# Kernel optimization log

Measured on AMD Instinct MI355X. Metric: run time of the kernel, lower is better.

The kernel has to match this reference:

```python
import jax, jax.numpy as jnp
import numpy as np


def conv3x3(x, w, b):
    # stride 1, pad 1, NCHW / OIHW
    out = jax.lax.conv_general_dilated(x, w, (1, 1), ((1, 1), (1, 1)),
                                       dimension_numbers=('NCHW', 'OIHW', 'NCHW'))
    return out + b[None, :, None, None]


def bilinear_sample(x, ys, xs):
    # x: [B,C,H,W]; ys,xs: [B,K,H,W] float sampling coords.
    # mmcv-style: zero outside image, per-corner validity.
    B, C, H, W = x.shape
    x_flat = x.reshape(B, C, H * W)
    y0 = jnp.floor(ys)
    x0 = jnp.floor(xs)
    dy = ys - y0
    dx = xs - x0
    y0i = y0.astype(jnp.int32)
    x0i = x0.astype(jnp.int32)

    def corner(yc, xc, wgt):
        valid = (yc >= 0) & (yc < H) & (xc >= 0) & (xc < W)
        idx = jnp.clip(yc, 0, H - 1) * W + jnp.clip(xc, 0, W - 1)  # [B,K,H,W]
        idx_f = idx.reshape(B, -1)
        vals = jax.vmap(lambda xf, ix: xf[:, ix])(x_flat, idx_f)  # [B,C,K*H*W]
        vals = vals.reshape(B, C, *yc.shape[1:])
        return vals * (wgt * valid)[:, None]

    out = corner(y0i, x0i, (1 - dy) * (1 - dx))
    out = out + corner(y0i, x0i + 1, (1 - dy) * dx)
    out = out + corner(y0i + 1, x0i, dy * (1 - dx))
    out = out + corner(y0i + 1, x0i + 1, dy * dx)
    return out  # [B,C,K,H,W]


def avgpool3s2(z):
    # AvgPool2d(kernel=3, stride=2, padding=1), count_include_pad=True -> divide by 9
    s = jax.lax.reduce_window(z, 0.0, jax.lax.add, (1, 1, 3, 3), (1, 1, 2, 2),
                              ((0, 0), (0, 0), (1, 1), (1, 1)))
    return s / 9.0


def setup_inputs() -> dict:
    key = jax.random.key(0)
    k1, k2, k3 = jax.random.split(key, 3)
    C = 64
    x = jax.random.normal(k1, (4, C, 128, 128), dtype=jnp.float32)
    w_off = jax.random.normal(k2, (27, C, 3, 3), dtype=jnp.float32) * 0.02
    b_off = jnp.zeros((27,), dtype=jnp.float32)
    w_align = jax.random.normal(k3, (C, C, 3, 3), dtype=jnp.float32) * 0.02
    b_align = jnp.zeros((C,), dtype=jnp.float32)
    return {"x": x, "w_off": w_off, "b_off": b_off, "w_align": w_align, "b_align": b_align}


def reference(x, w_off, b_off, w_align, b_align):
    B, C, H, W = x.shape
    K = 9
    off_all = conv3x3(x, w_off, b_off)               # [B,27,H,W]
    offset = off_all[:, :2 * K]                      # [B,18,H,W]
    mask = 2.0 * jax.nn.sigmoid(off_all[:, 2 * K:])  # [B,9,H,W]
    off = offset.reshape(B, K, 2, H, W)
    dy = off[:, :, 0]
    dx = off[:, :, 1]
    # base kernel grid (dilation 1, pad 1): offsets in {-1,0,1}
    ky = (jnp.arange(K) // 3 - 1).astype(jnp.float32)
    kx = (jnp.arange(K) % 3 - 1).astype(jnp.float32)
    ys = jnp.arange(H, dtype=jnp.float32)[None, None, :, None] + ky[None, :, None, None] + dy
    xs = jnp.arange(W, dtype=jnp.float32)[None, None, None, :] + kx[None, :, None, None] + dx
    sampled = bilinear_sample(x, ys, xs) * mask[:, None]    # [B,C,K,H,W]
    w = jnp.einsum('bckhw,ock->bohw', sampled, w_align.reshape(C, C, K))
    w = w + b_align[None, :, None, None]
    w = jnp.exp(jax.nn.sigmoid(w))
    return avgpool3s2(w * x) / avgpool3s2(w)
```

## Files before the change

### kernel.cpp

```cpp
#include <hip/hip_runtime.h>
#include <hip/hip_bf16.h>

#define HW 16384
#define CC 64
#define BB 4

typedef __attribute__((ext_vector_type(8))) short bf8;
typedef __attribute__((ext_vector_type(4))) float f4;

static __device__ __forceinline__ float bf2f(unsigned short u) {
    return __uint_as_float(((unsigned)u) << 16);
}
static __device__ __forceinline__ unsigned short f2bf(float f) {
    __hip_bfloat16 h = __float2bfloat16(f);
    return *reinterpret_cast<unsigned short*>(&h);
}

__global__ __launch_bounds__(256) void k_prep_tx(const float* __restrict__ x,
                                                 const float* __restrict__ w_off,
                                                 const float* __restrict__ w_align,
                                                 unsigned short* __restrict__ xT,
                                                 unsigned short* __restrict__ wA,
                                                 unsigned short* __restrict__ Wal) {
    __shared__ unsigned T32[64 * 33];
    int bx = blockIdx.x, t = threadIdx.x;
    if (bx < 216) {
        int i = bx * 256 + t;
        if (i < 32 * 576) {
            int m = i / 576, r = i - m * 576, tt = r >> 6, c = r & 63;
            float v = (m < 27) ? w_off[m * 576 + c * 9 + tt] : 0.f;
            wA[i] = f2bf(v);
        } else {
            int j = i - 32 * 576;
            int o = j / 576, r = j - o * 576, tt = r >> 6, c = r & 63;
            Wal[j] = f2bf(w_align[o * 576 + c * 9 + tt]);
        }
        return;
    }
    int pix0 = (bx - 216) * 64;
    int b = pix0 >> 14, hw0 = pix0 & (HW - 1);
    const float* xb = x + (size_t)b * CC * HW + hw0;
#pragma unroll
    for (int u = 0; u < 8; u++) {
        int i = t + 256 * u;
        int cp = i >> 6, p = i & 63;
        float v0 = xb[(size_t)(2 * cp) * HW + p];
        float v1 = xb[(size_t)(2 * cp + 1) * HW + p];
        T32[p * 33 + cp] = (unsigned)f2bf(v0) | ((unsigned)f2bf(v1) << 16);
    }
    __syncthreads();
#pragma unroll
    for (int u = 0; u < 2; u++) {
        int i = t + 256 * u;
        int p = i >> 3, q = i & 7;
        uint4 qq;
        qq.x = T32[p * 33 + q * 4 + 0];
        qq.y = T32[p * 33 + q * 4 + 1];
        qq.z = T32[p * 33 + q * 4 + 2];
        qq.w = T32[p * 33 + q * 4 + 3];
        *(uint4*)(xT + ((size_t)b * HW + hw0 + p) * CC + q * 8) = qq;
    }
}

__global__ __launch_bounds__(256, 4) void k_conv(const unsigned short* __restrict__ xT,
                                                 const unsigned short* __restrict__ wA,
                                                 const float* __restrict__ b_off,
                                                 float* __restrict__ off) {
    __shared__ __align__(16) unsigned short WL[32 * 584];
    int t = threadIdx.x, lane = t & 63, wv = t >> 6;
    int quad = lane >> 4, col = lane & 15;
#pragma unroll
    for (int u = 0; u < 9; u++) {
        int idx = t + 256 * u;
        int row = idx / 72, jb = idx - row * 72;
        *(uint4*)(WL + row * 584 + jb * 8) = ((const uint4*)wA)[idx];
    }
    __syncthreads();

    int n = blockIdx.x * 64 + wv * 16 + col;
    int b = n >> 14, hw = n & (HW - 1), h = hw >> 7, w = hw & 127;
    const unsigned short* xTb = xT + (size_t)b * HW * CC;
    const bf8 zero = {0, 0, 0, 0, 0, 0, 0, 0};

    f4 acc0 = {0.f, 0.f, 0.f, 0.f};
    f4 acc1 = {0.f, 0.f, 0.f, 0.f};
#pragma unroll
    for (int tap = 0; tap < 9; tap++) {
        int dyt = tap / 3 - 1, dxt = tap - (tap / 3) * 3 - 1;
        int hs = h + dyt, ws = w + dxt;
        bool valid = ((unsigned)hs < 128u) && ((unsigned)ws < 128u);
        int hc = min(max(hs, 0), 127), wc = min(max(ws, 0), 127);
        const unsigned short* src = xTb + ((size_t)(hc * 128 + wc)) * CC + quad * 8;
        bf8 b0 = *(const bf8*)(src);
        bf8 b1 = *(const bf8*)(src + 32);
        b0 = valid ? b0 : zero;
        b1 = valid ? b1 : zero;
        const unsigned short* l0 = WL + col * 584 + tap * 64 + quad * 8;
        const unsigned short* l1 = WL + (col + 16) * 584 + tap * 64 + quad * 8;
        acc0 = __builtin_amdgcn_mfma_f32_16x16x32_bf16(*(const bf8*)l0, b0, acc0, 0, 0, 0);
        acc1 = __builtin_amdgcn_mfma_f32_16x16x32_bf16(*(const bf8*)l1, b0, acc1, 0, 0, 0);
        acc0 = __builtin_amdgcn_mfma_f32_16x16x32_bf16(*(const bf8*)(l0 + 32), b1, acc0, 0, 0, 0);
        acc1 = __builtin_amdgcn_mfma_f32_16x16x32_bf16(*(const bf8*)(l1 + 32), b1, acc1, 0, 0, 0);
    }
#pragma unroll
    for (int i = 0; i < 4; i++) {
        int o0 = quad * 4 + i;
        {
            float v = acc0[i] + b_off[o0];
            if (o0 >= 18) v = 2.f / (1.f + __expf(-v));
            off[((size_t)b * 27 + o0) * HW + hw] = v;
        }
        int o1 = 16 + o0;
        if (o1 < 27) {
            float v = acc1[i] + b_off[o1];
            if (o1 >= 18) v = 2.f / (1.f + __expf(-v));
            off[((size_t)b * 27 + o1) * HW + hw] = v;
        }
    }
}

__global__ __launch_bounds__(256, 4) void k_fused(const unsigned short* __restrict__ xT,
                                                  const float* __restrict__ off,
                                                  const unsigned short* __restrict__ Wal,
                                                  const float* __restrict__ b_align,
                                                  float* __restrict__ wten) {
    __shared__ __align__(16) unsigned short WB[2][64 * 72];

    int t = threadIdx.x, lane = t & 63, wv = t >> 6;
    int quad = lane >> 4, col = lane & 15;
    int pix0 = blockIdx.x * 64;
    int b = pix0 >> 14;
    int px = (pix0 & (HW - 1)) + wv * 16 + col;
    int h = px >> 7, w = px & 127;
    const unsigned short* xTb = xT + (size_t)b * HW * CC;
    const float* offp = off + (size_t)b * 27 * HW + px;

    float dyv[9], dxv[9], mv[9];
#pragma unroll
    for (int k = 0; k < 9; k++) {
        dyv[k] = offp[(size_t)(2 * k) * HW];
        dxv[k] = offp[(size_t)(2 * k + 1) * HW];
        mv[k]  = offp[(size_t)(18 + k) * HW];
    }

#pragma unroll
    for (int u = 0; u < 2; u++) {
        int idx = t + 256 * u;
        int row = idx >> 3, jb = idx & 7;
        *(uint4*)(&WB[0][row * 72 + jb * 8]) = ((const uint4*)Wal)[row * 72 + jb];
    }
    __syncthreads();

    f4 acc[4];
#pragma unroll
    for (int mt = 0; mt < 4; mt++) acc[mt] = (f4){0.f, 0.f, 0.f, 0.f};

#pragma unroll
    for (int k = 0; k < 9; k++) {
        if (k < 8) {
#pragma unroll
            for (int u = 0; u < 2; u++) {
                int idx = t + 256 * u;
                int row = idx >> 3, jb = idx & 7;
                *(uint4*)(&WB[(k + 1) & 1][row * 72 + jb * 8]) =
                    ((const uint4*)Wal)[row * 72 + (k + 1) * 8 + jb];
            }
        }
        const unsigned short* WLg = WB[k & 1];

        float dy = dyv[k], dx = dxv[k], m = mv[k];
        int k3 = k / 3;
        float ys = (float)(h + k3 - 1) + dy;
        float xs = (float)(w + (k - 3 * k3) - 1) + dx;
        float y0f = floorf(ys), x0f = floorf(xs);
        float fy = ys - y0f, fx = xs - x0f;
        int y0 = (int)y0f, x0 = (int)x0f;
        int y1 = y0 + 1, x1 = x0 + 1;
        bool vy0 = (unsigned)y0 < 128u, vy1 = (unsigned)y1 < 128u;
        bool vx0 = (unsigned)x0 < 128u, vx1 = (unsigned)x1 < 128u;
        int cy0 = min(max(y0, 0), 127), cy1 = min(max(y1, 0), 127);
        int cx0 = min(max(x0, 0), 127), cx1 = min(max(x1, 0), 127);
        float w00 = (1.f - fy) * (1.f - fx) * ((vy0 && vx0) ? m : 0.f);
        float w01 = (1.f - fy) * fx         * ((vy0 && vx1) ? m : 0.f);
        float w10 = fy * (1.f - fx)         * ((vy1 && vx0) ? m : 0.f);
        float w11 = fy * fx                 * ((vy1 && vx1) ? m : 0.f);

        const unsigned short* c00 = xTb + ((size_t)(cy0 * 128 + cx0)) * CC + quad * 8;
        const unsigned short* c01 = xTb + ((size_t)(cy0 * 128 + cx1)) * CC + quad * 8;
        const unsigned short* c10 = xTb + ((size_t)(cy1 * 128 + cx0)) * CC + quad * 8;
        const unsigned short* c11 = xTb + ((size_t)(cy1 * 128 + cx1)) * CC + quad * 8;
        uint4 qa0 = *(const uint4*)(c00),      qa1 = *(const uint4*)(c01);
        uint4 qa2 = *(const uint4*)(c10),      qa3 = *(const uint4*)(c11);
        uint4 qb0 = *(const uint4*)(c00 + 32), qb1 = *(const uint4*)(c01 + 32);
        uint4 qb2 = *(const uint4*)(c10 + 32), qb3 = *(const uint4*)(c11 + 32);

        bf8 bfrag[2];
#pragma unroll
        for (int h2 = 0; h2 < 2; h2++) {
            const unsigned short* u00 = (const unsigned short*)(h2 ? &qb0 : &qa0);
            const unsigned short* u01 = (const unsigned short*)(h2 ? &qb1 : &qa1);
            const unsigned short* u10 = (const unsigned short*)(h2 ? &qb2 : &qa2);
            const unsigned short* u11 = (const unsigned short*)(h2 ? &qb3 : &qa3);
            unsigned short ov[8];
#pragma unroll
            for (int j = 0; j < 8; j++) {
                float v = w00 * bf2f(u00[j]) + w01 * bf2f(u01[j])
                        + w10 * bf2f(u10[j]) + w11 * bf2f(u11[j]);
                ov[j] = f2bf(v);
            }
            bfrag[h2] = *(const bf8*)ov;
        }
#pragma unroll
        for (int h2 = 0; h2 < 2; h2++) {
#pragma unroll
            for (int mt = 0; mt < 4; mt++) {
                const bf8 a = *(const bf8*)(WLg + (size_t)(mt * 16 + col) * 72
                                            + h2 * 32 + quad * 8);
                acc[mt] = __builtin_amdgcn_mfma_f32_16x16x32_bf16(a, bfrag[h2], acc[mt], 0, 0, 0);
            }
        }
        if (k < 8) __syncthreads();
    }

    float* wb = wten + (size_t)b * CC * HW + px;
#pragma unroll
    for (int mt = 0; mt < 4; mt++)
#pragma unroll
        for (int i = 0; i < 4; i++) {
            int o = mt * 16 + quad * 4 + i;
            float u = acc[mt][i] + b_align[o];
            float sg = 1.f / (1.f + __expf(-u));
            wb[(size_t)o * HW] = __expf(sg);
        }
}

__global__ __launch_bounds__(256) void k_pool(const float* __restrict__ x,
                                              const float* __restrict__ wten,
                                              float* __restrict__ out) {
    int idx = blockIdx.x * 256 + threadIdx.x;
    int ow = idx & 63;
    int oh = (idx >> 6) & 63;
    int bc = idx >> 12;
    const float* wp = wten + (size_t)bc * HW;
    const float* xp = x + (size_t)bc * HW;
    float num = 0.f, den = 0.f;
#pragma unroll
    for (int iy = 0; iy < 3; iy++) {
        int y = 2 * oh + iy - 1;
        if ((unsigned)y >= 128u) continue;
#pragma unroll
        for (int ix = 0; ix < 3; ix++) {
            int xc = 2 * ow + ix - 1;
            if ((unsigned)xc >= 128u) continue;
            float wv = wp[y * 128 + xc];
            float xv = xp[y * 128 + xc];
            num = fmaf(wv, xv, num);
            den += wv;
        }
    }
    out[idx] = num / den;
}

extern "C" void kernel_launch(void* const* d_in, const int* in_sizes, int n_in,
                              void* d_out, int out_size, void* d_ws, size_t ws_size,
                              hipStream_t stream) {
    const float* x       = (const float*)d_in[0];
    const float* w_off   = (const float*)d_in[1];
    const float* b_off   = (const float*)d_in[2];
    const float* w_align = (const float*)d_in[3];
    const float* b_align = (const float*)d_in[4];
    float* out = (float*)d_out;

    char* p = (char*)d_ws;
    float* off  = (float*)p;                  p += (size_t)BB * 27 * HW * 4;
    float* wten = (float*)p;                  p += (size_t)BB * CC * HW * 4;
    unsigned short* xT  = (unsigned short*)p; p += (size_t)BB * HW * CC * 2;
    unsigned short* wA  = (unsigned short*)p; p += 32 * 576 * 2;
    unsigned short* Wal = (unsigned short*)p;

    k_prep_tx<<<dim3(1240), dim3(256), 0, stream>>>(x, w_off, w_align, xT, wA, Wal);
    k_conv<<<dim3(1024), dim3(256), 0, stream>>>(xT, wA, b_off, off);
    k_fused<<<dim3(1024), dim3(256), 0, stream>>>(xT, off, Wal, b_align, wten);
    k_pool<<<dim3(4096), dim3(256), 0, stream>>>(x, wten, out);
}
```

Before: 131.2 us.

## Pre-swizzle align weights into MFMA fragment order and load directly from global

The align weights are rewritten during the prep kernel into per-lane MFMA A-fragment order, so each lane's 8 bf16 values sit contiguously. The fused kernel then reads A fragments straight from global memory (cached in L1/L2) instead of double-buffering them through shared memory. This removes the LDS staging stores and per-tap __syncthreads, and frees LDS for occupancy. The cost is more global and cache load traffic for each wave, since every block rereads the 72 KB weight set.

```diff
diff --git a/kernel.cpp b/kernel.cpp
--- a/kernel.cpp
+++ b/kernel.cpp
@@ -21,7 +21,7 @@
                                                  const float* __restrict__ w_align,
                                                  unsigned short* __restrict__ xT,
                                                  unsigned short* __restrict__ wA,
-                                                 unsigned short* __restrict__ Wal) {
+                                                 unsigned short* __restrict__ Wal2) {
     __shared__ unsigned T32[64 * 33];
     int bx = blockIdx.x, t = threadIdx.x;
     if (bx < 216) {
@@ -32,8 +32,17 @@
             wA[i] = f2bf(v);
         } else {
             int j = i - 32 * 576;
-            int o = j / 576, r = j - o * 576, tt = r >> 6, c = r & 63;
-            Wal[j] = f2bf(w_align[o * 576 + c * 9 + tt]);
+            int jj = j & 7;
+            int chunk = j >> 3;
+            int l = chunk & 63;
+            int g = chunk >> 6;
+            int mt = g & 3;
+            int th = g >> 2;
+            int h2 = th & 1;
+            int tp = th >> 1;
+            int o = mt * 16 + (l & 15);
+            int c = h2 * 32 + (l >> 4) * 8 + jj;
+            Wal2[j] = f2bf(w_align[o * 576 + c * 9 + tp]);
         }
         return;
     }
@@ -121,11 +130,9 @@
 
 __global__ __launch_bounds__(256, 4) void k_fused(const unsigned short* __restrict__ xT,
                                                   const float* __restrict__ off,
-                                                  const unsigned short* __restrict__ Wal,
+                                                  const unsigned short* __restrict__ Wal2,
                                                   const float* __restrict__ b_align,
                                                   float* __restrict__ wten) {
-    __shared__ __align__(16) unsigned short WB[2][64 * 72];
-
     int t = threadIdx.x, lane = t & 63, wv = t >> 6;
     int quad = lane >> 4, col = lane & 15;
     int pix0 = blockIdx.x * 64;
@@ -134,6 +141,7 @@
     int h = px >> 7, w = px & 127;
     const unsigned short* xTb = xT + (size_t)b * HW * CC;
     const float* offp = off + (size_t)b * 27 * HW + px;
+    const unsigned short* wl = Wal2 + lane * 8;
 
     float dyv[9], dxv[9], mv[9];
 #pragma unroll
@@ -143,31 +151,12 @@
         mv[k]  = offp[(size_t)(18 + k) * HW];
     }
 
-#pragma unroll
-    for (int u = 0; u < 2; u++) {
-        int idx = t + 256 * u;
-        int row = idx >> 3, jb = idx & 7;
-        *(uint4*)(&WB[0][row * 72 + jb * 8]) = ((const uint4*)Wal)[row * 72 + jb];
-    }
-    __syncthreads();
-
     f4 acc[4];
 #pragma unroll
     for (int mt = 0; mt < 4; mt++) acc[mt] = (f4){0.f, 0.f, 0.f, 0.f};
 
 #pragma unroll
     for (int k = 0; k < 9; k++) {
-        if (k < 8) {
-#pragma unroll
-            for (int u = 0; u < 2; u++) {
-                int idx = t + 256 * u;
-                int row = idx >> 3, jb = idx & 7;
-                *(uint4*)(&WB[(k + 1) & 1][row * 72 + jb * 8]) =
-                    ((const uint4*)Wal)[row * 72 + (k + 1) * 8 + jb];
-            }
-        }
-        const unsigned short* WLg = WB[k & 1];
-
         float dy = dyv[k], dx = dxv[k], m = mv[k];
         int k3 = k / 3;
         float ys = (float)(h + k3 - 1) + dy;
@@ -214,12 +203,10 @@
         for (int h2 = 0; h2 < 2; h2++) {
 #pragma unroll
             for (int mt = 0; mt < 4; mt++) {
-                const bf8 a = *(const bf8*)(WLg + (size_t)(mt * 16 + col) * 72
-                                            + h2 * 32 + quad * 8);
+                const bf8 a = *(const bf8*)(wl + (size_t)(((k * 2 + h2) * 4 + mt) * 512));
                 acc[mt] = __builtin_amdgcn_mfma_f32_16x16x32_bf16(a, bfrag[h2], acc[mt], 0, 0, 0);
             }
         }
-        if (k < 8) __syncthreads();
     }
 
     float* wb = wten + (size_t)b * CC * HW + px;
@@ -276,10 +263,10 @@
     float* wten = (float*)p;                  p += (size_t)BB * CC * HW * 4;
     unsigned short* xT  = (unsigned short*)p; p += (size_t)BB * HW * CC * 2;
     unsigned short* wA  = (unsigned short*)p; p += 32 * 576 * 2;
-    unsigned short* Wal = (unsigned short*)p;
-
-    k_prep_tx<<<dim3(1240), dim3(256), 0, stream>>>(x, w_off, w_align, xT, wA, Wal);
+    unsigned short* Wal2 = (unsigned short*)p;
+
+    k_prep_tx<<<dim3(1240), dim3(256), 0, stream>>>(x, w_off, w_align, xT, wA, Wal2);
     k_conv<<<dim3(1024), dim3(256), 0, stream>>>(xT, wA, b_off, off);
-    k_fused<<<dim3(1024), dim3(256), 0, stream>>>(xT, off, Wal, b_align, wten);
+    k_fused<<<dim3(1024), dim3(256), 0, stream>>>(xT, off, Wal2, b_align, wten);
     k_pool<<<dim3(4096), dim3(256), 0, stream>>>(x, wten, out);
 }
```

Measured after the change: 135.9 us. +3.6%, slower.
